# Kernel optimization log

Hardware: AMD Instinct MI355X
Metric: run time of the kernel (lower is better)

## Reference

```python
import jax, jax.numpy as jnp
import numpy as np

T = 4096
D = 512
H = 8
HD = D // H
DFF = D  # dim_ff = dmodel per module code
NUM_ACTIONS = 14
NUM_OBJECTS = 123
NEG = -1e9


def _layernorm(x, g, b, eps=1e-5):
    m = jnp.mean(x, axis=-1, keepdims=True)
    v = jnp.var(x, axis=-1, keepdims=True)
    return (x - m) / jnp.sqrt(v + eps) * g + b


def setup_inputs() -> dict:
    key = jax.random.key(0)
    ks = jax.random.split(key, 12)
    w = lambda k, s: (jax.random.normal(k, s) * 0.02).astype(jnp.float32)
    return {
        "action_seq": jax.random.randint(ks[0], (T, 2), 0, NUM_ACTIONS),
        "batch_id": jnp.sort(jax.random.randint(ks[1], (T,), 0, 16)),
        "W_type": w(ks[2], (NUM_ACTIONS, D)), "b_type": jnp.zeros((D,), jnp.float32),
        "W_arg": w(ks[3], (NUM_OBJECTS + 1, D)), "b_arg": jnp.zeros((D,), jnp.float32),
        "sos": jnp.zeros((D,), jnp.float32),
        "Wq": w(ks[4], (2, D, D)), "bq": jnp.zeros((2, D), jnp.float32),
        "Wk": w(ks[5], (2, D, D)), "bk": jnp.zeros((2, D), jnp.float32),
        "Wv": w(ks[6], (2, D, D)), "bv": jnp.zeros((2, D), jnp.float32),
        "Wo": w(ks[7], (2, D, D)), "bo": jnp.zeros((2, D), jnp.float32),
        "ln1_g": jnp.ones((2, D), jnp.float32), "ln1_b": jnp.zeros((2, D), jnp.float32),
        "W1": w(ks[8], (2, D, DFF)), "b1": jnp.zeros((2, DFF), jnp.float32),
        "W2": w(ks[9], (2, DFF, D)), "b2": jnp.zeros((2, D), jnp.float32),
        "ln2_g": jnp.ones((2, D), jnp.float32), "ln2_b": jnp.zeros((2, D), jnp.float32),
    }


def _forward(action_seq, batch_id, W_type, b_type, W_arg, b_arg, sos,
             Wq, bq, Wk, bk, Wv, bv, Wo, bo, ln1_g, ln1_b, W1, b1, W2, b2, ln2_g, ln2_b):
    Tn = action_seq.shape[0]
    dt = W_type.dtype
    # embeddings (one-hot @ W == Linear on one-hot)
    type_emb = jax.nn.one_hot(action_seq[:, 0], NUM_ACTIONS, dtype=dt) @ W_type + b_type
    arg_emb = jax.nn.one_hot(action_seq[:, 1] + 1, NUM_OBJECTS + 1, dtype=dt) @ W_arg + b_arg
    # position within each packed sequence (batch_id sorted-contiguous)
    seg_start = jnp.searchsorted(batch_id, batch_id, side='left')
    pos = (jnp.arange(Tn) - seg_start).astype(dt)
    div = jnp.exp(-jnp.log(10000.0) * jnp.arange(0, D, 2).astype(dt) / D)
    ang = pos[:, None] * div[None, :]
    pe = jnp.stack([jnp.sin(ang), jnp.cos(ang)], axis=-1).reshape(Tn, D)  # interleaved sin/cos
    x = jnp.concatenate([sos[None, :], type_emb + arg_emb + pe], axis=0)  # [T+1, D]
    T1 = Tn + 1
    # block-diagonal causal mask with prepended SOS token (always attendable)
    idx = jnp.arange(T1)
    bid1 = jnp.concatenate([jnp.full((1,), -1, dtype=batch_id.dtype), batch_id])
    allowed = (idx[:, None] >= idx[None, :]) & (bid1[:, None] == bid1[None, :])
    allowed = allowed | (idx[None, :] == 0)
    bias = jnp.where(allowed, 0.0, NEG).astype(dt)  # [T1, T1]
    scale = 1.0 / jnp.sqrt(jnp.asarray(HD, dtype=dt))
    for l in range(2):  # transformer_layer_a, transformer_layer_b
        q = (x @ Wq[l] + bq[l]).reshape(T1, H, HD)
        k = (x @ Wk[l] + bk[l]).reshape(T1, H, HD)
        v = (x @ Wv[l] + bv[l]).reshape(T1, H, HD)
        s = jnp.einsum('qhd,khd->hqk', q, k) * scale + bias[None, :, :]
        a = jax.nn.softmax(s, axis=-1)
        o = jnp.einsum('hqk,khd->qhd', a, v).reshape(T1, D) @ Wo[l] + bo[l]
        x = _layernorm(x + o, ln1_g[l], ln1_b[l])
        f = jax.nn.relu(x @ W1[l] + b1[l]) @ W2[l] + b2[l]
        x = _layernorm(x + f, ln2_g[l], ln2_b[l])
    return x  # [T+1, D]


def reference(action_seq, batch_id, W_type, b_type, W_arg, b_arg, sos,
              Wq, bq, Wk, bk, Wv, bv, Wo, bo, ln1_g, ln1_b, W1, b1, W2, b2, ln2_g, ln2_b):
    return _forward(action_seq, batch_id, W_type, b_type, W_arg, b_arg, sos,
                    Wq, bq, Wk, bk, Wv, bv, Wo, bo, ln1_g, ln1_b, W1, b1, W2, b2, ln2_g, ln2_b)
```

## Files before the change

kernel.cpp:

```cpp
#include <hip/hip_runtime.h>
#include <hip/hip_bf16.h>
#include <stdint.h>

#define T_TOK 4096
#define T1N   4097
#define DMODEL 512
#define VTS   4160

typedef __attribute__((ext_vector_type(8))) short bf16x8;
typedef __attribute__((ext_vector_type(4))) float f32x4;

static __device__ __forceinline__ unsigned short f2bf(float f) {
  __hip_bfloat16 h = __float2bfloat16(f);
  return *reinterpret_cast<unsigned short*>(&h);
}

static __device__ __forceinline__ void stage_tile(
    const __hip_bfloat16* __restrict__ src, __hip_bfloat16* lds,
    int row0, int k0, int srcld, int maxrow, int wave, int lane) {
  #pragma unroll
  for (int i = 0; i < 2; i++) {
    int row = wave*8 + i*32 + (lane>>3);
    int grow = row0 + row; if (grow > maxrow) grow = maxrow;
    const __hip_bfloat16* g = src + (size_t)grow*srcld + k0 + (lane&7)*8;
    __hip_bfloat16* l = lds + (wave*8 + i*32)*64;
    __builtin_amdgcn_global_load_lds(
        (const __attribute__((address_space(1))) void*)g,
        (__attribute__((address_space(3))) void*)l, 16, 0, 0);
  }
}

__global__ __launch_bounds__(256) void prep_kernel(
    const int* __restrict__ aseq, const int* __restrict__ bid,
    const float* __restrict__ Wt, const float* __restrict__ bt,
    const float* __restrict__ Wa, const float* __restrict__ ba,
    const float* __restrict__ sosv,
    const float* __restrict__ Wq, const float* __restrict__ Wk,
    const float* __restrict__ Wv, const float* __restrict__ Wo,
    const float* __restrict__ W1, const float* __restrict__ W2,
    float* __restrict__ x, __hip_bfloat16* __restrict__ xb,
    int* __restrict__ ss, __hip_bfloat16* __restrict__ wtout) {
  __shared__ float tile[32][33];
  const int b = blockIdx.x;
  const int tid = threadIdx.x;
  if (b < T1N) {
    int i = b;
    int d0 = tid * 2;
    float o0, o1;
    if (i == 0) {
      o0 = sosv[d0]; o1 = sosv[d0+1];
    } else {
      int t = i - 1;
      int a0 = aseq[2*t], a1 = aseq[2*t+1];
      int key = bid[t];
      int lo = 0, hi = t;
      while (lo < hi) { int mid = (lo+hi) >> 1; if (bid[mid] < key) lo = mid + 1; else hi = mid; }
      if (tid == 0) ss[t] = lo;
      float pos = (float)(t - lo);
      float dv = __expf(-9.210340371976184f * (float)d0 * (1.0f/(float)DMODEL));
      float ang = pos * dv;
      float sn = sinf(ang), cs = cosf(ang);
      o0 = Wt[(size_t)a0*DMODEL + d0]   + bt[d0]   + Wa[(size_t)(a1+1)*DMODEL + d0]   + ba[d0]   + sn;
      o1 = Wt[(size_t)a0*DMODEL + d0+1] + bt[d0+1] + Wa[(size_t)(a1+1)*DMODEL + d0+1] + ba[d0+1] + cs;
    }
    size_t base = (size_t)i*DMODEL + d0;
    x[base] = o0; x[base+1] = o1;
    xb[base] = __float2bfloat16(o0); xb[base+1] = __float2bfloat16(o1);
  } else {
    int w = b - T1N;
    int m = w >> 8;
    int rem = w & 255;
    int bn = (rem >> 4) * 32;
    int bk = (rem & 15) * 32;
    int kind = m >> 1, layer = m & 1;
    const float* src = kind==0?Wq: kind==1?Wk: kind==2?Wv: kind==3?Wo: kind==4?W1:W2;
    src += (size_t)layer*DMODEL*DMODEL;
    __hip_bfloat16* dst = wtout + (size_t)m*DMODEL*DMODEL;
    int tx = tid & 31, ty = tid >> 5;
    for (int r = ty; r < 32; r += 8)
      tile[r][tx] = src[(size_t)(bk + r)*DMODEL + bn + tx];
    __syncthreads();
    for (int r = ty; r < 32; r += 8)
      dst[(size_t)(bn + r)*DMODEL + bk + tx] = __float2bfloat16(tile[tx][r]);
  }
}

template<int ACT, bool WF32, bool WB16>
__global__ __launch_bounds__(256) void gemm_one(
    const __hip_bfloat16* __restrict__ A, const __hip_bfloat16* __restrict__ Bt,
    const float* __restrict__ bias, float* __restrict__ Cf,
    __hip_bfloat16* __restrict__ Cb, int M) {
  constexpr int K = 512, N = 512;
  __shared__ __align__(16) __hip_bfloat16 As[64*64];
  __shared__ __align__(16) __hip_bfloat16 Bs[64*64];
  const int tid = threadIdx.x;
  const int m0 = blockIdx.x * 64;
  const int n0 = blockIdx.y * 64;
  const int lane = tid & 63, wave = tid >> 6;
  const int wm = wave >> 1, wn = wave & 1;
  f32x4 acc[2][2] = {};
  for (int k0 = 0; k0 < K; k0 += 64) {
    __syncthreads();
    stage_tile(A,  As, m0, k0, K, M-1, wave, lane);
    stage_tile(Bt, Bs, n0, k0, K, N-1, wave, lane);
    __syncthreads();
    #pragma unroll
    for (int kc = 0; kc < 64; kc += 32) {
      bf16x8 af[2], bf[2];
      #pragma unroll
      for (int i2 = 0; i2 < 2; i2++) {
        af[i2] = *(const bf16x8*)&As[(wm*32 + i2*16 + (lane&15))*64 + kc + (lane>>4)*8];
        bf[i2] = *(const bf16x8*)&Bs[(wn*32 + i2*16 + (lane&15))*64 + kc + (lane>>4)*8];
      }
      #pragma unroll
      for (int mi = 0; mi < 2; mi++)
        #pragma unroll
        for (int ni = 0; ni < 2; ni++)
          acc[mi][ni] = __builtin_amdgcn_mfma_f32_16x16x32_bf16(af[mi], bf[ni], acc[mi][ni], 0, 0, 0);
    }
  }
  #pragma unroll
  for (int mi = 0; mi < 2; mi++) {
    int rbase = m0 + wm*32 + mi*16 + ((lane>>4)<<2);
    #pragma unroll
    for (int ni = 0; ni < 2; ni++) {
      int col = n0 + wn*32 + ni*16 + (lane&15);
      float bb = bias[col];
      #pragma unroll
      for (int r = 0; r < 4; r++) {
        int row = rbase + r;
        if (row < M) {
          float val = acc[mi][ni][r] + bb;
          if (ACT == 1) val = fmaxf(val, 0.0f);
          if (WF32) Cf[(size_t)row*N + col] = val;
          if (WB16) Cb[(size_t)row*N + col] = __float2bfloat16(val);
        }
      }
    }
  }
}

__global__ __launch_bounds__(256) void gemm_qkv(
    const __hip_bfloat16* __restrict__ A,
    const __hip_bfloat16* __restrict__ B0, const __hip_bfloat16* __restrict__ B1,
    const __hip_bfloat16* __restrict__ B2,
    const float* __restrict__ bias0, const float* __restrict__ bias1, const float* __restrict__ bias2,
    __hip_bfloat16* __restrict__ C0, __hip_bfloat16* __restrict__ C1, __hip_bfloat16* __restrict__ vt,
    int M) {
  constexpr int K = 512;
  __shared__ __align__(16) __hip_bfloat16 As[64*64];
  __shared__ __align__(16) __hip_bfloat16 Bs[3][64*64];
  const int tid = threadIdx.x;
  const int m0 = blockIdx.x * 64;
  const int n0 = blockIdx.y * 64;
  const int lane = tid & 63, wave = tid >> 6;
  const int wm = wave >> 1, wn = wave & 1;
  f32x4 acc[3][2][2] = {};
  for (int k0 = 0; k0 < K; k0 += 64) {
    __syncthreads();
    stage_tile(A,  As,    m0, k0, K, M-1, wave, lane);
    stage_tile(B0, Bs[0], n0, k0, K, 511, wave, lane);
    stage_tile(B1, Bs[1], n0, k0, K, 511, wave, lane);
    stage_tile(B2, Bs[2], n0, k0, K, 511, wave, lane);
    __syncthreads();
    #pragma unroll
    for (int kc = 0; kc < 64; kc += 32) {
      bf16x8 af[2];
      #pragma unroll
      for (int i2 = 0; i2 < 2; i2++)
        af[i2] = *(const bf16x8*)&As[(wm*32 + i2*16 + (lane&15))*64 + kc + (lane>>4)*8];
      #pragma unroll
      for (int z = 0; z < 3; z++) {
        bf16x8 bf[2];
        #pragma unroll
        for (int i2 = 0; i2 < 2; i2++)
          bf[i2] = *(const bf16x8*)&Bs[z][(wn*32 + i2*16 + (lane&15))*64 + kc + (lane>>4)*8];
        #pragma unroll
        for (int i = 0; i < 2; i++)
          #pragma unroll
          for (int j = 0; j < 2; j++) {
            if (z == 2) acc[2][i][j] = __builtin_amdgcn_mfma_f32_16x16x32_bf16(bf[i], af[j], acc[2][i][j], 0, 0, 0);
            else        acc[z][i][j] = __builtin_amdgcn_mfma_f32_16x16x32_bf16(af[i], bf[j], acc[z][i][j], 0, 0, 0);
          }
      }
    }
  }
  #pragma unroll
  for (int z = 0; z < 2; z++) {
    __hip_bfloat16* Cz = (z==0) ? C0 : C1;
    const float* bz = (z==0) ? bias0 : bias1;
    #pragma unroll
    for (int mi = 0; mi < 2; mi++) {
      int rbase = m0 + wm*32 + mi*16 + ((lane>>4)<<2);
      #pragma unroll
      for (int ni = 0; ni < 2; ni++) {
        int col = n0 + wn*32 + ni*16 + (lane&15);
        float bb = bz[col];
        #pragma unroll
        for (int r = 0; r < 4; r++) {
          int row = rbase + r;
          if (row < M) Cz[(size_t)row*DMODEL + col] = __float2bfloat16(acc[z][mi][ni][r] + bb);
        }
      }
    }
  }
  #pragma unroll
  for (int bi = 0; bi < 2; bi++) {
    int rbase = n0 + wn*32 + bi*16 + ((lane>>4)<<2);
    #pragma unroll
    for (int ai = 0; ai < 2; ai++) {
      int colm = m0 + wm*32 + ai*16 + (lane&15);
      if (colm < M) {
        #pragma unroll
        for (int r = 0; r < 4; r++) {
          int rn = rbase + r;
          vt[(size_t)rn*VTS + colm] = __float2bfloat16(acc[2][bi][ai][r] + bias2[rn]);
        }
      }
    }
  }
}

__global__ __launch_bounds__(64) void attn_kernel(
    const __hip_bfloat16* __restrict__ q,
    const __hip_bfloat16* __restrict__ k,
    const __hip_bfloat16* __restrict__ vt,
    const int* __restrict__ ss,
    __hip_bfloat16* __restrict__ out) {
  const int h  = blockIdx.y;
  const int q0 = blockIdx.x * 16;
  const int lane = threadIdx.x;
  const int g  = lane >> 4;
  const int qi = lane & 15;
  const int qrow = q0 + qi;

  int qld = (qrow < T1N) ? qrow : (T1N-1);
  const __hip_bfloat16* qp = q + (size_t)qld*DMODEL + h*64 + g*8;
  bf16x8 qlo = *(const bf16x8*)qp;
  bf16x8 qhi = *(const bf16x8*)(qp + 32);

  int jl;
  if (qrow >= T1N)      jl = 0x7fffffff;
  else if (qrow == 0)   jl = 1;
  else                  jl = ss[qrow-1] + 1;

  const __hip_bfloat16* k0p = k + h*64 + g*8;
  float part = 0.0f;
  #pragma unroll
  for (int e = 0; e < 8; e++) {
    part += __bfloat162float(((const __hip_bfloat16*)&qlo)[e]) * __bfloat162float(k0p[e]);
    part += __bfloat162float(((const __hip_bfloat16*)&qhi)[e]) * __bfloat162float(k0p[e+32]);
  }
  part += __shfl_xor(part, 16);
  part += __shfl_xor(part, 32);
  float m = part * 0.125f;
  float lsum = 1.0f;
  f32x4 o[4];
  #pragma unroll
  for (int d = 0; d < 4; d++) {
    float v0 = __bfloat162float(vt[(size_t)(h*64 + d*16 + qi)*VTS]);
    o[d] = (f32x4){v0, v0, v0, v0};
  }

  const int mjl = (q0 == 0) ? 1 : (ss[q0-1] + 1);
  const int kb_lo = mjl & ~31;
  const int jmax = (q0 + 15 < T1N - 1) ? (q0 + 15) : (T1N - 1);

  const int src0 = ((g & 1) << 5) + qi;
  const bool hiHalf = (g >= 2);

  bf16x8 cka0, cka1, ckb0, ckb1, cv0, cv1, cv2, cv3;
  {
    int kr0 = kb_lo + qi;       if (kr0 > T1N-1) kr0 = T1N-1;
    int kr1 = kb_lo + 16 + qi;  if (kr1 > T1N-1) kr1 = T1N-1;
    const __hip_bfloat16* kp0 = k + (size_t)kr0*DMODEL + h*64 + g*8;
    const __hip_bfloat16* kp1 = k + (size_t)kr1*DMODEL + h*64 + g*8;
    cka0 = *(const bf16x8*)kp0; cka1 = *(const bf16x8*)(kp0 + 32);
    ckb0 = *(const bf16x8*)kp1; ckb1 = *(const bf16x8*)(kp1 + 32);
    const __hip_bfloat16* vp = vt + (size_t)(h*64 + qi)*VTS + kb_lo + g*8;
    cv0 = *(const bf16x8*)vp;
    cv1 = *(const bf16x8*)(vp + (size_t)16*VTS);
    cv2 = *(const bf16x8*)(vp + (size_t)32*VTS);
    cv3 = *(const bf16x8*)(vp + (size_t)48*VTS);
  }

  for (int kbb = kb_lo; kbb <= jmax; kbb += 32) {
    int kn = (kbb + 32 <= jmax) ? (kbb + 32) : kbb;
    bf16x8 nka0, nka1, nkb0, nkb1, nv0, nv1, nv2, nv3;
    {
      int kr0 = kn + qi;       if (kr0 > T1N-1) kr0 = T1N-1;
      int kr1 = kn + 16 + qi;  if (kr1 > T1N-1) kr1 = T1N-1;
      const __hip_bfloat16* kp0 = k + (size_t)kr0*DMODEL + h*64 + g*8;
      const __hip_bfloat16* kp1 = k + (size_t)kr1*DMODEL + h*64 + g*8;
      nka0 = *(const bf16x8*)kp0; nka1 = *(const bf16x8*)(kp0 + 32);
      nkb0 = *(const bf16x8*)kp1; nkb1 = *(const bf16x8*)(kp1 + 32);
      const __hip_bfloat16* vp = vt + (size_t)(h*64 + qi)*VTS + kn + g*8;
      nv0 = *(const bf16x8*)vp;
      nv1 = *(const bf16x8*)(vp + (size_t)16*VTS);
      nv2 = *(const bf16x8*)(vp + (size_t)32*VTS);
      nv3 = *(const bf16x8*)(vp + (size_t)48*VTS);
    }

    f32x4 sA = {0,0,0,0}, sB = {0,0,0,0};
    sA = __builtin_amdgcn_mfma_f32_16x16x32_bf16(cka0, qlo, sA, 0, 0, 0);
    sA = __builtin_amdgcn_mfma_f32_16x16x32_bf16(cka1, qhi, sA, 0, 0, 0);
    sB = __builtin_amdgcn_mfma_f32_16x16x32_bf16(ckb0, qlo, sB, 0, 0, 0);
    sB = __builtin_amdgcn_mfma_f32_16x16x32_bf16(ckb1, qhi, sB, 0, 0, 0);

    float s[8];
    const int kA = kbb + 4*g, kB = kA + 16;
    #pragma unroll
    for (int r = 0; r < 4; r++) {
      s[r]   = (kA + r >= jl && kA + r <= qrow) ? sA[r]*0.125f : -1e30f;
      s[4+r] = (kB + r >= jl && kB + r <= qrow) ? sB[r]*0.125f : -1e30f;
    }
    float mx = s[0];
    #pragma unroll
    for (int i = 1; i < 8; i++) mx = fmaxf(mx, s[i]);
    mx = fmaxf(mx, __shfl_xor(mx, 16));
    mx = fmaxf(mx, __shfl_xor(mx, 32));
    float mnew = fmaxf(m, mx);
    float corr = __expf(m - mnew);
    m = mnew;
    float p[8], psum = 0.0f;
    #pragma unroll
    for (int i = 0; i < 8; i++) { p[i] = __expf(s[i] - mnew); psum += p[i]; }
    psum += __shfl_xor(psum, 16);
    psum += __shfl_xor(psum, 32);
    lsum = lsum*corr + psum;

    bf16x8 pa;
    #pragma unroll
    for (int r = 0; r < 4; r++) {
      unsigned w = (unsigned)f2bf(p[r]) | ((unsigned)f2bf(p[4+r]) << 16);
      unsigned v0 = (unsigned)__shfl((int)w, src0);
      unsigned v1 = (unsigned)__shfl((int)w, src0 + 16);
      pa[r]     = (short)(hiHalf ? (v0 >> 16) : (v0 & 0xffff));
      pa[4 + r] = (short)(hiHalf ? (v1 >> 16) : (v1 & 0xffff));
    }

    float cq0 = __shfl(corr, 4*g + 0);
    float cq1 = __shfl(corr, 4*g + 1);
    float cq2 = __shfl(corr, 4*g + 2);
    float cq3 = __shfl(corr, 4*g + 3);
    f32x4 cqv = (f32x4){cq0, cq1, cq2, cq3};
    #pragma unroll
    for (int d = 0; d < 4; d++) o[d] *= cqv;

    o[0] = __builtin_amdgcn_mfma_f32_16x16x32_bf16(pa, cv0, o[0], 0, 0, 0);
    o[1] = __builtin_amdgcn_mfma_f32_16x16x32_bf16(pa, cv1, o[1], 0, 0, 0);
    o[2] = __builtin_amdgcn_mfma_f32_16x16x32_bf16(pa, cv2, o[2], 0, 0, 0);
    o[3] = __builtin_amdgcn_mfma_f32_16x16x32_bf16(pa, cv3, o[3], 0, 0, 0);

    cka0 = nka0; cka1 = nka1; ckb0 = nkb0; ckb1 = nkb1;
    cv0 = nv0; cv1 = nv1; cv2 = nv2; cv3 = nv3;
  }

  float inv = 1.0f / lsum;
  float li0 = __shfl(inv, 4*g + 0);
  float li1 = __shfl(inv, 4*g + 1);
  float li2 = __shfl(inv, 4*g + 2);
  float li3 = __shfl(inv, 4*g + 3);
  f32x4 liv = (f32x4){li0, li1, li2, li3};
  #pragma unroll
  for (int r = 0; r < 4; r++) {
    int row = q0 + 4*g + r;
    if (row < T1N) {
      __hip_bfloat16* op = out + (size_t)row*DMODEL + h*64 + qi;
      #pragma unroll
      for (int d = 0; d < 4; d++) op[d*16] = __float2bfloat16(o[d][r] * liv[r]);
    }
  }
}

__global__ __launch_bounds__(256) void ln_kernel(
    const float* __restrict__ xin, const float* __restrict__ yin,
    const float* __restrict__ g, const float* __restrict__ b,
    float* __restrict__ xout, __hip_bfloat16* __restrict__ xbout) {
  int row = blockIdx.x;
  int tid = threadIdx.x;
  const float* xp = xin + (size_t)row*DMODEL;
  const float* yp = yin + (size_t)row*DMODEL;
  float2 xv = *(const float2*)(xp + tid*2);
  float2 yv = *(const float2*)(yp + tid*2);
  float v0 = xv.x + yv.x;
  float v1 = xv.y + yv.y;
  float s = v0 + v1, sq = v0*v0 + v1*v1;
  #pragma unroll
  for (int off = 1; off < 64; off <<= 1) {
    s  += __shfl_xor(s, off);
    sq += __shfl_xor(sq, off);
  }
  __shared__ float ls[4], lq[4];
  int wave = tid >> 6;
  if ((tid & 63) == 0) { ls[wave] = s; lq[wave] = sq; }
  __syncthreads();
  s  = ls[0] + ls[1] + ls[2] + ls[3];
  sq = lq[0] + lq[1] + lq[2] + lq[3];
  float mean = s * (1.0f/512.0f);
  float var  = sq * (1.0f/512.0f) - mean*mean;
  float rstd = rsqrtf(var + 1e-5f);
  float g0 = g[tid*2], g1 = g[tid*2+1];
  float b0 = b[tid*2], b1 = b[tid*2+1];
  float o0 = (v0 - mean)*rstd*g0 + b0;
  float o1 = (v1 - mean)*rstd*g1 + b1;
  size_t base = (size_t)row*DMODEL + tid*2;
  *(float2*)(xout + base) = make_float2(o0, o1);
  xbout[base]   = __float2bfloat16(o0);
  xbout[base+1] = __float2bfloat16(o1);
}

extern "C" void kernel_launch(void* const* d_in, const int* in_sizes, int n_in,
                              void* d_out, int out_size, void* d_ws, size_t ws_size,
                              hipStream_t stream) {
  const int*   aseq   = (const int*)d_in[0];
  const int*   bid    = (const int*)d_in[1];
  const float* W_type = (const float*)d_in[2];
  const float* b_type = (const float*)d_in[3];
  const float* W_arg  = (const float*)d_in[4];
  const float* b_arg  = (const float*)d_in[5];
  const float* sosv   = (const float*)d_in[6];
  const float* Wq = (const float*)d_in[7];
  const float* bq = (const float*)d_in[8];
  const float* Wk = (const float*)d_in[9];
  const float* bk = (const float*)d_in[10];
  const float* Wv = (const float*)d_in[11];
  const float* bv = (const float*)d_in[12];
  const float* Wo = (const float*)d_in[13];
  const float* bo = (const float*)d_in[14];
  const float* ln1g = (const float*)d_in[15];
  const float* ln1b = (const float*)d_in[16];
  const float* W1 = (const float*)d_in[17];
  const float* b1 = (const float*)d_in[18];
  const float* W2 = (const float*)d_in[19];
  const float* b2 = (const float*)d_in[20];
  const float* ln2g = (const float*)d_in[21];
  const float* ln2b = (const float*)d_in[22];

  char* wsp = (char*)d_ws;
  size_t off = 0;
  auto alloc = [&](size_t bytes) -> void* {
    void* p = wsp + off; off += (bytes + 255) & ~(size_t)255; return p;
  };
  __hip_bfloat16* WT  = (__hip_bfloat16*)alloc((size_t)12*512*512*2);
  float* x            = (float*)alloc((size_t)T1N*DMODEL*4);
  __hip_bfloat16* xb  = (__hip_bfloat16*)alloc((size_t)T1N*DMODEL*2);
  __hip_bfloat16* qb  = (__hip_bfloat16*)alloc((size_t)T1N*DMODEL*2);
  __hip_bfloat16* kbf = (__hip_bfloat16*)alloc((size_t)T1N*DMODEL*2);
  __hip_bfloat16* vtb = (__hip_bfloat16*)alloc((size_t)512*VTS*2);
  float* y            = (float*)alloc((size_t)T1N*DMODEL*4);
  __hip_bfloat16* ab  = (__hip_bfloat16*)alloc((size_t)T1N*DMODEL*2);
  __hip_bfloat16* f1b = (__hip_bfloat16*)alloc((size_t)T1N*DMODEL*2);
  int* ss             = (int*)alloc((size_t)T_TOK*4);

  prep_kernel<<<dim3(T1N + 12*256), 256, 0, stream>>>(
      aseq, bid, W_type, b_type, W_arg, b_arg, sosv,
      Wq, Wk, Wv, Wo, W1, W2, x, xb, ss, WT);

  const size_t WSZ = (size_t)512*512;
  const dim3 ggrid(65, 8);
  for (int l = 0; l < 2; l++) {
    const __hip_bfloat16* Bq  = WT + (size_t)(0*2+l)*WSZ;
    const __hip_bfloat16* Bk  = WT + (size_t)(1*2+l)*WSZ;
    const __hip_bfloat16* Bv  = WT + (size_t)(2*2+l)*WSZ;
    const __hip_bfloat16* Bo  = WT + (size_t)(3*2+l)*WSZ;
    const __hip_bfloat16* Bf1 = WT + (size_t)(4*2+l)*WSZ;
    const __hip_bfloat16* Bf2 = WT + (size_t)(5*2+l)*WSZ;

    gemm_qkv<<<ggrid, 256, 0, stream>>>(xb, Bq, Bk, Bv,
        bq + l*512, bk + l*512, bv + l*512, qb, kbf, vtb, T1N);
    attn_kernel<<<dim3(257,8), 64, 0, stream>>>(qb, kbf, vtb, ss, ab);
    gemm_one<0,true,false><<<ggrid, 256, 0, stream>>>(ab, Bo, bo + l*512, y, nullptr, T1N);
    ln_kernel<<<dim3(T1N), 256, 0, stream>>>(x, y, ln1g + l*512, ln1b + l*512, x, xb);
    gemm_one<1,false,true><<<ggrid, 256, 0, stream>>>(xb, Bf1, b1 + l*512, nullptr, f1b, T1N);
    gemm_one<0,true,false><<<ggrid, 256, 0, stream>>>(f1b, Bf2, b2 + l*512, y, nullptr, T1N);
    float* xout = (l == 1) ? (float*)d_out : x;
    ln_kernel<<<dim3(T1N), 256, 0, stream>>>(x, y, ln2g + l*512, ln2b + l*512, xout, xb);
  }
}
```

Baseline: 205.1 us.

## Double-buffer GEMM LDS tiles and store GEMM outputs for layernorm in bf16

Both GEMM kernels now use two LDS buffers, so the global loads for the next K tile are issued before the MFMA work on the current tile, with one barrier per iteration instead of two. The Wo and W2 projection outputs feeding layernorm are written as bf16 instead of fp32, which halves that intermediate traffic. The cost is twice the LDS per block (about 64KB for the QKV kernel), which may lower occupancy, plus some added rounding in the residual branch.

```diff
diff --git a/kernel.cpp b/kernel.cpp
--- a/kernel.cpp
+++ b/kernel.cpp
@@ -85,32 +85,36 @@
   }
 }
 
-template<int ACT, bool WF32, bool WB16>
+template<int ACT>
 __global__ __launch_bounds__(256) void gemm_one(
     const __hip_bfloat16* __restrict__ A, const __hip_bfloat16* __restrict__ Bt,
-    const float* __restrict__ bias, float* __restrict__ Cf,
-    __hip_bfloat16* __restrict__ Cb, int M) {
+    const float* __restrict__ bias, __hip_bfloat16* __restrict__ Cb, int M) {
   constexpr int K = 512, N = 512;
-  __shared__ __align__(16) __hip_bfloat16 As[64*64];
-  __shared__ __align__(16) __hip_bfloat16 Bs[64*64];
+  __shared__ __align__(16) __hip_bfloat16 As[2][64*64];
+  __shared__ __align__(16) __hip_bfloat16 Bs[2][64*64];
   const int tid = threadIdx.x;
   const int m0 = blockIdx.x * 64;
   const int n0 = blockIdx.y * 64;
   const int lane = tid & 63, wave = tid >> 6;
   const int wm = wave >> 1, wn = wave & 1;
   f32x4 acc[2][2] = {};
-  for (int k0 = 0; k0 < K; k0 += 64) {
-    __syncthreads();
-    stage_tile(A,  As, m0, k0, K, M-1, wave, lane);
-    stage_tile(Bt, Bs, n0, k0, K, N-1, wave, lane);
-    __syncthreads();
+  stage_tile(A,  As[0], m0, 0, K, M-1, wave, lane);
+  stage_tile(Bt, Bs[0], n0, 0, K, N-1, wave, lane);
+  __syncthreads();
+  #pragma unroll
+  for (int t = 0; t < 8; ++t) {
+    const int cb = t & 1;
+    if (t < 7) {
+      stage_tile(A,  As[cb^1], m0, (t+1)*64, K, M-1, wave, lane);
+      stage_tile(Bt, Bs[cb^1], n0, (t+1)*64, K, N-1, wave, lane);
+    }
     #pragma unroll
     for (int kc = 0; kc < 64; kc += 32) {
       bf16x8 af[2], bf[2];
       #pragma unroll
       for (int i2 = 0; i2 < 2; i2++) {
-        af[i2] = *(const bf16x8*)&As[(wm*32 + i2*16 + (lane&15))*64 + kc + (lane>>4)*8];
-        bf[i2] = *(const bf16x8*)&Bs[(wn*32 + i2*16 + (lane&15))*64 + kc + (lane>>4)*8];
+        af[i2] = *(const bf16x8*)&As[cb][(wm*32 + i2*16 + (lane&15))*64 + kc + (lane>>4)*8];
+        bf[i2] = *(const bf16x8*)&Bs[cb][(wn*32 + i2*16 + (lane&15))*64 + kc + (lane>>4)*8];
       }
       #pragma unroll
       for (int mi = 0; mi < 2; mi++)
@@ -118,6 +122,7 @@
         for (int ni = 0; ni < 2; ni++)
           acc[mi][ni] = __builtin_amdgcn_mfma_f32_16x16x32_bf16(af[mi], bf[ni], acc[mi][ni], 0, 0, 0);
     }
+    __syncthreads();
   }
   #pragma unroll
   for (int mi = 0; mi < 2; mi++) {
@@ -132,8 +137,7 @@
         if (row < M) {
           float val = acc[mi][ni][r] + bb;
           if (ACT == 1) val = fmaxf(val, 0.0f);
-          if (WF32) Cf[(size_t)row*N + col] = val;
-          if (WB16) Cb[(size_t)row*N + col] = __float2bfloat16(val);
+          Cb[(size_t)row*N + col] = __float2bfloat16(val);
         }
       }
     }
@@ -148,33 +152,41 @@
     __hip_bfloat16* __restrict__ C0, __hip_bfloat16* __restrict__ C1, __hip_bfloat16* __restrict__ vt,
     int M) {
   constexpr int K = 512;
-  __shared__ __align__(16) __hip_bfloat16 As[64*64];
-  __shared__ __align__(16) __hip_bfloat16 Bs[3][64*64];
+  __shared__ __align__(16) __hip_bfloat16 As[2][64*64];
+  __shared__ __align__(16) __hip_bfloat16 Bs[2][3][64*64];
   const int tid = threadIdx.x;
   const int m0 = blockIdx.x * 64;
   const int n0 = blockIdx.y * 64;
   const int lane = tid & 63, wave = tid >> 6;
   const int wm = wave >> 1, wn = wave & 1;
   f32x4 acc[3][2][2] = {};
-  for (int k0 = 0; k0 < K; k0 += 64) {
-    __syncthreads();
-    stage_tile(A,  As,    m0, k0, K, M-1, wave, lane);
-    stage_tile(B0, Bs[0], n0, k0, K, 511, wave, lane);
-    stage_tile(B1, Bs[1], n0, k0, K, 511, wave, lane);
-    stage_tile(B2, Bs[2], n0, k0, K, 511, wave, lane);
-    __syncthreads();
+  stage_tile(A,  As[0],    m0, 0, K, M-1, wave, lane);
+  stage_tile(B0, Bs[0][0], n0, 0, K, 511, wave, lane);
+  stage_tile(B1, Bs[0][1], n0, 0, K, 511, wave, lane);
+  stage_tile(B2, Bs[0][2], n0, 0, K, 511, wave, lane);
+  __syncthreads();
+  #pragma unroll
+  for (int t = 0; t < 8; ++t) {
+    const int cb = t & 1;
+    if (t < 7) {
+      const int k0n = (t+1)*64;
+      stage_tile(A,  As[cb^1],    m0, k0n, K, M-1, wave, lane);
+      stage_tile(B0, Bs[cb^1][0], n0, k0n, K, 511, wave, lane);
+      stage_tile(B1, Bs[cb^1][1], n0, k0n, K, 511, wave, lane);
+      stage_tile(B2, Bs[cb^1][2], n0, k0n, K, 511, wave, lane);
+    }
     #pragma unroll
     for (int kc = 0; kc < 64; kc += 32) {
       bf16x8 af[2];
       #pragma unroll
       for (int i2 = 0; i2 < 2; i2++)
-        af[i2] = *(const bf16x8*)&As[(wm*32 + i2*16 + (lane&15))*64 + kc + (lane>>4)*8];
+        af[i2] = *(const bf16x8*)&As[cb][(wm*32 + i2*16 + (lane&15))*64 + kc + (lane>>4)*8];
       #pragma unroll
       for (int z = 0; z < 3; z++) {
         bf16x8 bf[2];
         #pragma unroll
         for (int i2 = 0; i2 < 2; i2++)
-          bf[i2] = *(const bf16x8*)&Bs[z][(wn*32 + i2*16 + (lane&15))*64 + kc + (lane>>4)*8];
+          bf[i2] = *(const bf16x8*)&Bs[cb][z][(wn*32 + i2*16 + (lane&15))*64 + kc + (lane>>4)*8];
         #pragma unroll
         for (int i = 0; i < 2; i++)
           #pragma unroll
@@ -184,6 +196,7 @@
           }
       }
     }
+    __syncthreads();
   }
   #pragma unroll
   for (int z = 0; z < 2; z++) {
@@ -374,17 +387,17 @@
 }
 
 __global__ __launch_bounds__(256) void ln_kernel(
-    const float* __restrict__ xin, const float* __restrict__ yin,
+    const float* __restrict__ xin, const __hip_bfloat16* __restrict__ yin,
     const float* __restrict__ g, const float* __restrict__ b,
     float* __restrict__ xout, __hip_bfloat16* __restrict__ xbout) {
   int row = blockIdx.x;
   int tid = threadIdx.x;
-  const float* xp = xin + (size_t)row*DMODEL;
-  const float* yp = yin + (size_t)row*DMODEL;
-  float2 xv = *(const float2*)(xp + tid*2);
-  float2 yv = *(const float2*)(yp + tid*2);
-  float v0 = xv.x + yv.x;
-  float v1 = xv.y + yv.y;
+  float2 xv = *(const float2*)(xin + (size_t)row*DMODEL + tid*2);
+  unsigned yw = *(const unsigned*)(yin + (size_t)row*DMODEL + tid*2);
+  float y0 = __bfloat162float(((const __hip_bfloat16*)&yw)[0]);
+  float y1 = __bfloat162float(((const __hip_bfloat16*)&yw)[1]);
+  float v0 = xv.x + y0;
+  float v1 = xv.y + y1;
   float s = v0 + v1, sq = v0*v0 + v1*v1;
   #pragma unroll
   for (int off = 1; off < 64; off <<= 1) {
@@ -448,7 +461,7 @@
   __hip_bfloat16* qb  = (__hip_bfloat16*)alloc((size_t)T1N*DMODEL*2);
   __hip_bfloat16* kbf = (__hip_bfloat16*)alloc((size_t)T1N*DMODEL*2);
   __hip_bfloat16* vtb = (__hip_bfloat16*)alloc((size_t)512*VTS*2);
-  float* y            = (float*)alloc((size_t)T1N*DMODEL*4);
+  __hip_bfloat16* yb  = (__hip_bfloat16*)alloc((size_t)T1N*DMODEL*2);
   __hip_bfloat16* ab  = (__hip_bfloat16*)alloc((size_t)T1N*DMODEL*2);
   __hip_bfloat16* f1b = (__hip_bfloat16*)alloc((size_t)T1N*DMODEL*2);
   int* ss             = (int*)alloc((size_t)T_TOK*4);
@@ -470,11 +483,11 @@
     gemm_qkv<<<ggrid, 256, 0, stream>>>(xb, Bq, Bk, Bv,
         bq + l*512, bk + l*512, bv + l*512, qb, kbf, vtb, T1N);
     attn_kernel<<<dim3(257,8), 64, 0, stream>>>(qb, kbf, vtb, ss, ab);
-    gemm_one<0,true,false><<<ggrid, 256, 0, stream>>>(ab, Bo, bo + l*512, y, nullptr, T1N);
-    ln_kernel<<<dim3(T1N), 256, 0, stream>>>(x, y, ln1g + l*512, ln1b + l*512, x, xb);
-    gemm_one<1,false,true><<<ggrid, 256, 0, stream>>>(xb, Bf1, b1 + l*512, nullptr, f1b, T1N);
-    gemm_one<0,true,false><<<ggrid, 256, 0, stream>>>(f1b, Bf2, b2 + l*512, y, nullptr, T1N);
+    gemm_one<0><<<ggrid, 256, 0, stream>>>(ab, Bo, bo + l*512, yb, T1N);
+    ln_kernel<<<dim3(T1N), 256, 0, stream>>>(x, yb, ln1g + l*512, ln1b + l*512, x, xb);
+    gemm_one<1><<<ggrid, 256, 0, stream>>>(xb, Bf1, b1 + l*512, f1b, T1N);
+    gemm_one<0><<<ggrid, 256, 0, stream>>>(f1b, Bf2, b2 + l*512, yb, T1N);
     float* xout = (l == 1) ? (float*)d_out : x;
-    ln_kernel<<<dim3(T1N), 256, 0, stream>>>(x, y, ln2g + l*512, ln2b + l*512, xout, xb);
-  }
-}
+    ln_kernel<<<dim3(T1N), 256, 0, stream>>>(x, yb, ln2g + l*512, ln2b + l*512, xout, xb);
+  }
+}
```

Result: slower. 209.3 us (+2.1%).
